# Kernel optimization log

Measured on AMD Instinct MI355X. Metric: run time of the kernel, lower is better.

## Reference

```python
import jax, jax.numpy as jnp
import numpy as np

VOCAB, D, PAD, SPARSITY = 6, 32, 5, 0.15


def setup_inputs() -> dict:
    key = jax.random.key(0)
    ks = jax.random.split(key, 16)
    x = jax.random.randint(ks[0], (256, 4096), 0, VOCAB, dtype=jnp.int32)
    s = 0.1
    emb = jax.random.normal(ks[1], (VOCAB, D), jnp.float32) * s
    return {
        "x": x,
        "emb": emb,
        # selector: D -> D//2 -> 1 (sigmoid)
        "sel_w1": jax.random.normal(ks[2], (D, D // 2), jnp.float32) * s,
        "sel_b1": jnp.zeros((D // 2,), jnp.float32),
        "sel_w2": jax.random.normal(ks[3], (D // 2, 1), jnp.float32) * s,
        "sel_b2": jnp.zeros((1,), jnp.float32),
        # approximator: D -> D -> D
        "app_w1": jax.random.normal(ks[4], (D, D), jnp.float32) * s,
        "app_b1": jnp.zeros((D,), jnp.float32),
        "app_w2": jax.random.normal(ks[5], (D, D), jnp.float32) * s,
        "app_b2": jnp.zeros((D,), jnp.float32),
        # classifier: D -> D//2 -> 1 (sigmoid)
        "cls_w1": jax.random.normal(ks[6], (D, D // 2), jnp.float32) * s,
        "cls_b1": jnp.zeros((D // 2,), jnp.float32),
        "cls_w2": jax.random.normal(ks[7], (D // 2, 1), jnp.float32) * s,
        "cls_b2": jnp.zeros((1,), jnp.float32),
    }


def reference(x, emb, sel_w1, sel_b1, sel_w2, sel_b2,
              app_w1, app_b1, app_w2, app_b2,
              cls_w1, cls_b1, cls_w2, cls_b2):
    B, S = x.shape
    k = max(1, int(S * SPARSITY))
    table = emb.at[PAD].set(0.0)            # padding_idx row is zero
    e = table[x]                            # [B, S, D]
    # selector scores (tiny MLP + sigmoid)
    h = jax.nn.relu(e @ sel_w1 + sel_b1)
    scores = jax.nn.sigmoid((h @ sel_w2 + sel_b2).squeeze(-1))  # [B, S]
    _, top_idx = jax.lax.top_k(scores, k)   # [B, k]
    sel = jnp.take_along_axis(e, top_idx[..., None], axis=1)    # [B, k, D]
    a = jax.nn.relu(sel @ app_w1 + app_b1) @ app_w2 + app_b2    # [B, k, D]
    pooled = a.mean(axis=1)                 # [B, D]
    c = jax.nn.relu(pooled @ cls_w1 + cls_b1)
    pred = jax.nn.sigmoid((c @ cls_w2 + cls_b2).squeeze(-1))    # [B]
    return pred, top_idx, scores
```

## Files before the change

kernel.cpp:

```cpp
#include <hip/hip_runtime.h>
#include <math.h>

#define VOCABN 6
#define DIM 32
#define PADI 5
#define BATCH 256
#define SEQ 4096
#define KSEL 614

__device__ __forceinline__ float lut6(float s0, float s1, float s2, float s3,
                                      float s4, float s5, int tk) {
    float r = s0;
    r = (tk == 1) ? s1 : r;
    r = (tk == 2) ? s2 : r;
    r = (tk == 3) ? s3 : r;
    r = (tk == 4) ? s4 : r;
    r = (tk == 5) ? s5 : r;
    return r;
}

__global__ __launch_bounds__(1024) void fused_row_kernel(
    const int* __restrict__ x,
    const float* __restrict__ emb,
    const float* __restrict__ sel_w1, const float* __restrict__ sel_b1,
    const float* __restrict__ sel_w2, const float* __restrict__ sel_b2,
    const float* __restrict__ app_w1, const float* __restrict__ app_b1,
    const float* __restrict__ app_w2, const float* __restrict__ app_b2,
    const float* __restrict__ cls_w1, const float* __restrict__ cls_b1,
    const float* __restrict__ cls_w2, const float* __restrict__ cls_b2,
    float* __restrict__ out_pred,
    float* __restrict__ out_topidx,
    float* __restrict__ out_scores) {
    const int b = blockIdx.x;
    const int t = threadIdx.x;
    const int lane = t & 63;
    const int w = t >> 6;

    __shared__ float s_emb[VOCABN * DIM];
    __shared__ float s_selw1[DIM * (DIM / 2)];
    __shared__ float s_selb1[DIM / 2], s_selw2[DIM / 2];
    __shared__ float s_selb2, s_clsb2v;
    __shared__ float s_appw1[DIM * DIM];
    __shared__ float s_appw2[DIM * DIM];
    __shared__ float s_appb1[DIM], s_appb2[DIM];
    __shared__ float s_clsw1[DIM * (DIM / 2)];
    __shared__ float s_clsb1[DIM / 2], s_clsw2[DIM / 2];
    __shared__ int s_wtot[16][VOCABN];

    const int4 tw = *(const int4*)(x + (size_t)b * SEQ + t * 4);

    s_appw1[t] = app_w1[t];
    s_appw2[t] = app_w2[t];
    if (t < 512) s_selw1[t] = sel_w1[t];
    else s_clsw1[t - 512] = cls_w1[t - 512];
    if (t < 192) s_emb[t] = (t >= PADI * DIM) ? 0.f : emb[t];
    else if (t < 208) { int i = t - 192; s_selb1[i] = sel_b1[i]; }
    else if (t < 224) { int i = t - 208; s_selw2[i] = sel_w2[i]; }
    else if (t < 256) { int i = t - 224; s_appb1[i] = app_b1[i]; }
    else if (t < 288) { int i = t - 256; s_appb2[i] = app_b2[i]; }
    else if (t < 304) { int i = t - 288; s_clsb1[i] = cls_b1[i]; }
    else if (t < 320) { int i = t - 304; s_clsw2[i] = cls_w2[i]; }
    else if (t == 320) s_selb2 = sel_b2[0];
    else if (t == 321) s_clsb2v = cls_b2[0];

    int tok[4];
    tok[0] = tw.x; tok[1] = tw.y; tok[2] = tw.z; tok[3] = tw.w;

    int cnt[VOCABN], val[VOCABN];
    #pragma unroll
    for (int v = 0; v < VOCABN; ++v) {
        int c = 0;
        #pragma unroll
        for (int i = 0; i < 4; ++i) c += (tok[i] == v) ? 1 : 0;
        cnt[v] = c; val[v] = c;
    }
    for (int off = 1; off < 64; off <<= 1) {
        #pragma unroll
        for (int v = 0; v < VOCABN; ++v) {
            int up = __shfl_up(val[v], off, 64);
            if (lane >= off) val[v] += up;
        }
    }
    if (lane == 63) {
        #pragma unroll
        for (int v = 0; v < VOCABN; ++v) s_wtot[w][v] = val[v];
    }

    __syncthreads();

    int sv = lane >> 3; if (sv >= VOCABN) sv -= VOCABN;
    const int j0 = (lane & 7) * 2;
    float h0 = s_selb1[j0], h1 = s_selb1[j0 + 1];
    #pragma unroll
    for (int d = 0; d < DIM; ++d) {
        const float e = s_emb[sv * DIM + d];
        h0 += e * s_selw1[d * (DIM / 2) + j0];
        h1 += e * s_selw1[d * (DIM / 2) + j0 + 1];
    }
    float part = fmaxf(h0, 0.f) * s_selw2[j0] + fmaxf(h1, 0.f) * s_selw2[j0 + 1];
    part += __shfl_xor(part, 1, 64);
    part += __shfl_xor(part, 2, 64);
    part += __shfl_xor(part, 4, 64);
    const float sig = 1.f / (1.f + expf(-(part + s_selb2)));
    const float sc0 = __shfl(sig,  0, 64);
    const float sc1 = __shfl(sig,  8, 64);
    const float sc2 = __shfl(sig, 16, 64);
    const float sc3 = __shfl(sig, 24, 64);
    const float sc4 = __shfl(sig, 32, 64);
    const float sc5 = __shfl(sig, 40, 64);

    {
        float4 f;
        f.x = lut6(sc0, sc1, sc2, sc3, sc4, sc5, tok[0]);
        f.y = lut6(sc0, sc1, sc2, sc3, sc4, sc5, tok[1]);
        f.z = lut6(sc0, sc1, sc2, sc3, sc4, sc5, tok[2]);
        f.w = lut6(sc0, sc1, sc2, sc3, sc4, sc5, tok[3]);
        *(float4*)(out_scores + (size_t)b * SEQ + t * 4) = f;
    }

    const float scv[VOCABN] = {sc0, sc1, sc2, sc3, sc4, sc5};
    int totv[VOCABN];
    #pragma unroll
    for (int v = 0; v < VOCABN; ++v) {
        int tot = 0;
        for (int ww = 0; ww < 16; ++ww) tot += s_wtot[ww][v];
        totv[v] = tot;
    }
    int rk[VOCABN];
    #pragma unroll
    for (int v = 0; v < VOCABN; ++v) {
        int r = 0;
        #pragma unroll
        for (int u = 0; u < VOCABN; ++u) {
            if (scv[u] > scv[v]) ++r;
            else if (scv[u] == scv[v] && u < v) ++r;
        }
        rk[v] = r;
    }
    int selv[VOCABN], basev[VOCABN];
    #pragma unroll
    for (int v = 0; v < VOCABN; ++v) {
        int before = 0;
        #pragma unroll
        for (int u = 0; u < VOCABN; ++u) before += (rk[u] < rk[v]) ? totv[u] : 0;
        const int base = before < KSEL ? before : KSEL;
        int take = KSEL - base;
        take = totv[v] < take ? totv[v] : take;
        basev[v] = base;
        selv[v] = take > 0 ? take : 0;
    }

    int excl[VOCABN];
    #pragma unroll
    for (int v = 0; v < VOCABN; ++v) {
        int pre = 0;
        for (int ww = 0; ww < w; ++ww) pre += s_wtot[ww][v];
        excl[v] = pre + val[v] - cnt[v];
    }
    #pragma unroll
    for (int v = 0; v < VOCABN; ++v) {
        int p = excl[v];
        #pragma unroll
        for (int i = 0; i < 4; ++i) {
            if (tok[i] == v) {
                if (p < selv[v]) out_topidx[(size_t)b * KSEL + basev[v] + p] = (float)(t * 4 + i);
                ++p;
            }
        }
    }

    if (w == 1) {
        float pooled = 0.f;
        #pragma unroll
        for (int v = 0; v < VOCABN; ++v) {
            float ah = 0.f;
            if (lane < DIM) {
                ah = s_appb1[lane];
                #pragma unroll
                for (int d = 0; d < DIM; ++d) ah += s_emb[v * DIM + d] * s_appw1[d * DIM + lane];
                ah = fmaxf(ah, 0.f);
            }
            float av = (lane < DIM) ? s_appb2[lane] : 0.f;
            #pragma unroll
            for (int j = 0; j < DIM; ++j) {
                const float ahj = __shfl(ah, j, 64);
                if (lane < DIM) av += ahj * s_appw2[j * DIM + lane];
            }
            pooled += (float)selv[v] * av;
        }
        pooled *= (1.f / (float)KSEL);
        float c = (lane < DIM / 2) ? s_clsb1[lane] : 0.f;
        #pragma unroll
        for (int d = 0; d < DIM; ++d) {
            const float pd = __shfl(pooled, d, 64);
            if (lane < DIM / 2) c += pd * s_clsw1[d * (DIM / 2) + lane];
        }
        float term = (lane < DIM / 2) ? fmaxf(c, 0.f) * s_clsw2[lane] : 0.f;
        term += __shfl_xor(term, 1, 64);
        term += __shfl_xor(term, 2, 64);
        term += __shfl_xor(term, 4, 64);
        term += __shfl_xor(term, 8, 64);
        if (lane == 0) out_pred[b] = 1.f / (1.f + expf(-(term + s_clsb2v)));
    }
}

extern "C" void kernel_launch(void* const* d_in, const int* in_sizes, int n_in,
                              void* d_out, int out_size, void* d_ws, size_t ws_size,
                              hipStream_t stream) {
    const int*   x      = (const int*)  d_in[0];
    const float* emb    = (const float*)d_in[1];
    const float* sel_w1 = (const float*)d_in[2];
    const float* sel_b1 = (const float*)d_in[3];
    const float* sel_w2 = (const float*)d_in[4];
    const float* sel_b2 = (const float*)d_in[5];
    const float* app_w1 = (const float*)d_in[6];
    const float* app_b1 = (const float*)d_in[7];
    const float* app_w2 = (const float*)d_in[8];
    const float* app_b2 = (const float*)d_in[9];
    const float* cls_w1 = (const float*)d_in[10];
    const float* cls_b1 = (const float*)d_in[11];
    const float* cls_w2 = (const float*)d_in[12];
    const float* cls_b2 = (const float*)d_in[13];

    float* out = (float*)d_out;
    float* out_pred   = out;
    float* out_topidx = out + BATCH;
    float* out_scores = out + BATCH + BATCH * KSEL;

    fused_row_kernel<<<BATCH, 1024, 0, stream>>>(
        x, emb, sel_w1, sel_b1, sel_w2, sel_b2,
        app_w1, app_b1, app_w2, app_b2,
        cls_w1, cls_b1, cls_w2, cls_b2,
        out_pred, out_topidx, out_scores);
}
```

Measured before the change: 99.42 us.

## Split per-row selection bookkeeping across specialized wavefronts with shared-memory handoff

Score computation, rank/base calculation, and the per-wave prefix sums are now done once by dedicated wavefronts and published through shared memory, instead of every thread redundantly computing them. Hidden-layer approximator activations are computed in parallel by three waves and the output projection by a separate wave, with the pooled vote split across both half-waves. Scores are gathered via a shared-memory table lookup instead of a select chain. This adds a second block-wide barrier in exchange for removing redundant per-thread serial loops over warps.

```diff
diff --git a/kernel.cpp b/kernel.cpp
--- a/kernel.cpp
+++ b/kernel.cpp
@@ -7,17 +7,6 @@
 #define BATCH 256
 #define SEQ 4096
 #define KSEL 614
-
-__device__ __forceinline__ float lut6(float s0, float s1, float s2, float s3,
-                                      float s4, float s5, int tk) {
-    float r = s0;
-    r = (tk == 1) ? s1 : r;
-    r = (tk == 2) ? s2 : r;
-    r = (tk == 3) ? s3 : r;
-    r = (tk == 4) ? s4 : r;
-    r = (tk == 5) ? s5 : r;
-    return r;
-}
 
 __global__ __launch_bounds__(1024) void fused_row_kernel(
     const int* __restrict__ x,
@@ -45,7 +34,11 @@
     __shared__ float s_appb1[DIM], s_appb2[DIM];
     __shared__ float s_clsw1[DIM * (DIM / 2)];
     __shared__ float s_clsb1[DIM / 2], s_clsw2[DIM / 2];
+    __shared__ float s_ah[VOCABN * DIM];
+    __shared__ float s_score[VOCABN];
     __shared__ int s_wtot[16][VOCABN];
+    __shared__ int s_wpre[16][VOCABN];
+    __shared__ int s_selbase[VOCABN];
 
     const int4 tw = *(const int4*)(x + (size_t)b * SEQ + t * 4);
 
@@ -88,107 +81,120 @@
 
     __syncthreads();
 
-    int sv = lane >> 3; if (sv >= VOCABN) sv -= VOCABN;
-    const int j0 = (lane & 7) * 2;
-    float h0 = s_selb1[j0], h1 = s_selb1[j0 + 1];
-    #pragma unroll
-    for (int d = 0; d < DIM; ++d) {
-        const float e = s_emb[sv * DIM + d];
-        h0 += e * s_selw1[d * (DIM / 2) + j0];
-        h1 += e * s_selw1[d * (DIM / 2) + j0 + 1];
-    }
-    float part = fmaxf(h0, 0.f) * s_selw2[j0] + fmaxf(h1, 0.f) * s_selw2[j0 + 1];
-    part += __shfl_xor(part, 1, 64);
-    part += __shfl_xor(part, 2, 64);
-    part += __shfl_xor(part, 4, 64);
-    const float sig = 1.f / (1.f + expf(-(part + s_selb2)));
-    const float sc0 = __shfl(sig,  0, 64);
-    const float sc1 = __shfl(sig,  8, 64);
-    const float sc2 = __shfl(sig, 16, 64);
-    const float sc3 = __shfl(sig, 24, 64);
-    const float sc4 = __shfl(sig, 32, 64);
-    const float sc5 = __shfl(sig, 40, 64);
+    if (w == 0) {
+        int sv = lane >> 3; if (sv >= VOCABN) sv -= VOCABN;
+        const int j0 = (lane & 7) * 2;
+        const float2 bj = *(const float2*)(s_selb1 + j0);
+        const float2 wj = *(const float2*)(s_selw2 + j0);
+        float h0 = bj.x, h1 = bj.y;
+        #pragma unroll
+        for (int d = 0; d < DIM; ++d) {
+            const float e = s_emb[sv * DIM + d];
+            const float2 ww = *(const float2*)(s_selw1 + d * (DIM / 2) + j0);
+            h0 += e * ww.x;
+            h1 += e * ww.y;
+        }
+        float part = fmaxf(h0, 0.f) * wj.x + fmaxf(h1, 0.f) * wj.y;
+        part += __shfl_xor(part, 1, 64);
+        part += __shfl_xor(part, 2, 64);
+        part += __shfl_xor(part, 4, 64);
+        const float sig = 1.f / (1.f + expf(-(part + s_selb2)));
+        float scv[VOCABN];
+        #pragma unroll
+        for (int v = 0; v < VOCABN; ++v) scv[v] = __shfl(sig, v * 8, 64);
+        if (lane < VOCABN) s_score[lane] = scv[lane];
+
+        int tv[VOCABN];
+        #pragma unroll
+        for (int v = 0; v < VOCABN; ++v) tv[v] = s_wtot[lane & 15][v];
+        #pragma unroll
+        for (int m = 1; m <= 8; m <<= 1) {
+            #pragma unroll
+            for (int v = 0; v < VOCABN; ++v) tv[v] += __shfl_xor(tv[v], m, 64);
+        }
+        int rk[VOCABN];
+        #pragma unroll
+        for (int v = 0; v < VOCABN; ++v) {
+            int r = 0;
+            #pragma unroll
+            for (int u = 0; u < VOCABN; ++u) {
+                if (scv[u] > scv[v]) ++r;
+                else if (scv[u] == scv[v] && u < v) ++r;
+            }
+            rk[v] = r;
+        }
+        if (lane < VOCABN) {
+            const int v = lane;
+            int before = 0;
+            #pragma unroll
+            for (int u = 0; u < VOCABN; ++u) before += (rk[u] < rk[v]) ? tv[u] : 0;
+            const int base = before < KSEL ? before : KSEL;
+            int take = KSEL - base;
+            take = tv[v] < take ? tv[v] : take;
+            take = take > 0 ? take : 0;
+            s_selbase[v] = take | (base << 16);
+        }
+    } else if (w == 1) {
+        int tv[VOCABN], inc[VOCABN];
+        #pragma unroll
+        for (int v = 0; v < VOCABN; ++v) { tv[v] = s_wtot[lane & 15][v]; inc[v] = tv[v]; }
+        #pragma unroll
+        for (int off = 1; off <= 8; off <<= 1) {
+            #pragma unroll
+            for (int v = 0; v < VOCABN; ++v) {
+                int up = __shfl_up(inc[v], off, 64);
+                if ((lane & 15) >= off) inc[v] += up;
+            }
+        }
+        if (lane < 16) {
+            #pragma unroll
+            for (int v = 0; v < VOCABN; ++v) s_wpre[lane][v] = inc[v] - tv[v];
+        }
+    } else if (w >= 2 && w < 5) {
+        const int i = t - 128, v = i >> 5, j = i & 31;
+        float acc = s_appb1[j];
+        #pragma unroll
+        for (int d = 0; d < DIM; ++d) acc += s_emb[v * DIM + d] * s_appw1[d * DIM + j];
+        s_ah[i] = fmaxf(acc, 0.f);
+    }
+
+    __syncthreads();
 
     {
         float4 f;
-        f.x = lut6(sc0, sc1, sc2, sc3, sc4, sc5, tok[0]);
-        f.y = lut6(sc0, sc1, sc2, sc3, sc4, sc5, tok[1]);
-        f.z = lut6(sc0, sc1, sc2, sc3, sc4, sc5, tok[2]);
-        f.w = lut6(sc0, sc1, sc2, sc3, sc4, sc5, tok[3]);
+        f.x = s_score[tok[0]]; f.y = s_score[tok[1]];
+        f.z = s_score[tok[2]]; f.w = s_score[tok[3]];
         *(float4*)(out_scores + (size_t)b * SEQ + t * 4) = f;
     }
 
-    const float scv[VOCABN] = {sc0, sc1, sc2, sc3, sc4, sc5};
-    int totv[VOCABN];
     #pragma unroll
     for (int v = 0; v < VOCABN; ++v) {
-        int tot = 0;
-        for (int ww = 0; ww < 16; ++ww) tot += s_wtot[ww][v];
-        totv[v] = tot;
-    }
-    int rk[VOCABN];
-    #pragma unroll
-    for (int v = 0; v < VOCABN; ++v) {
-        int r = 0;
-        #pragma unroll
-        for (int u = 0; u < VOCABN; ++u) {
-            if (scv[u] > scv[v]) ++r;
-            else if (scv[u] == scv[v] && u < v) ++r;
-        }
-        rk[v] = r;
-    }
-    int selv[VOCABN], basev[VOCABN];
-    #pragma unroll
-    for (int v = 0; v < VOCABN; ++v) {
-        int before = 0;
-        #pragma unroll
-        for (int u = 0; u < VOCABN; ++u) before += (rk[u] < rk[v]) ? totv[u] : 0;
-        const int base = before < KSEL ? before : KSEL;
-        int take = KSEL - base;
-        take = totv[v] < take ? totv[v] : take;
-        basev[v] = base;
-        selv[v] = take > 0 ? take : 0;
-    }
-
-    int excl[VOCABN];
-    #pragma unroll
-    for (int v = 0; v < VOCABN; ++v) {
-        int pre = 0;
-        for (int ww = 0; ww < w; ++ww) pre += s_wtot[ww][v];
-        excl[v] = pre + val[v] - cnt[v];
-    }
-    #pragma unroll
-    for (int v = 0; v < VOCABN; ++v) {
-        int p = excl[v];
+        const int sb = s_selbase[v];
+        const int sel = sb & 0xffff;
+        const int bs = sb >> 16;
+        int p = s_wpre[w][v] + val[v] - cnt[v];
         #pragma unroll
         for (int i = 0; i < 4; ++i) {
             if (tok[i] == v) {
-                if (p < selv[v]) out_topidx[(size_t)b * KSEL + basev[v] + p] = (float)(t * 4 + i);
+                if (p < sel) out_topidx[(size_t)b * KSEL + bs + p] = (float)(t * 4 + i);
                 ++p;
             }
         }
     }
 
-    if (w == 1) {
-        float pooled = 0.f;
-        #pragma unroll
-        for (int v = 0; v < VOCABN; ++v) {
-            float ah = 0.f;
-            if (lane < DIM) {
-                ah = s_appb1[lane];
-                #pragma unroll
-                for (int d = 0; d < DIM; ++d) ah += s_emb[v * DIM + d] * s_appw1[d * DIM + lane];
-                ah = fmaxf(ah, 0.f);
-            }
-            float av = (lane < DIM) ? s_appb2[lane] : 0.f;
-            #pragma unroll
-            for (int j = 0; j < DIM; ++j) {
-                const float ahj = __shfl(ah, j, 64);
-                if (lane < DIM) av += ahj * s_appw2[j * DIM + lane];
-            }
-            pooled += (float)selv[v] * av;
-        }
-        pooled *= (1.f / (float)KSEL);
+    if (w == 5) {
+        const int j = lane & 31;
+        const int half = lane >> 5;
+        float part = 0.f;
+        #pragma unroll
+        for (int r = 0; r < 3; ++r) {
+            const int v = 2 * r + half;
+            float av = s_appb2[j];
+            #pragma unroll
+            for (int k = 0; k < DIM; ++k) av += s_ah[v * DIM + k] * s_appw2[k * DIM + j];
+            part += (float)(s_selbase[v] & 0xffff) * av;
+        }
+        float pooled = (part + __shfl_xor(part, 32, 64)) * (1.f / (float)KSEL);
         float c = (lane < DIM / 2) ? s_clsb1[lane] : 0.f;
         #pragma unroll
         for (int d = 0; d < DIM; ++d) {
```

Result: faster. 89.33 us (-10.1%).
